# Kernel optimization log

Measured on AMD Instinct MI355X. Metric: run time of the kernel, lower is better.

Reference implementation:

```python
import jax, jax.numpy as jnp
import numpy as np

DIM = 512
B, H_GRID, W_GRID = 16, 64, 64
N_TOKENS = 1 + H_GRID * W_GRID


def setup_inputs() -> dict:
    key = jax.random.key(0)
    ks = jax.random.split(key, 7)
    x = jax.random.normal(ks[0], (B, N_TOKENS, DIM), dtype=jnp.float32)
    # depthwise conv weights, torch layout [C_out, C_in/groups=1, k, k]
    w7 = jax.random.normal(ks[1], (DIM, 1, 7, 7), dtype=jnp.float32) * 0.02
    b7 = jax.random.normal(ks[2], (DIM,), dtype=jnp.float32) * 0.02
    w5 = jax.random.normal(ks[3], (DIM, 1, 5, 5), dtype=jnp.float32) * 0.02
    b5 = jax.random.normal(ks[4], (DIM,), dtype=jnp.float32) * 0.02
    w3 = jax.random.normal(ks[5], (DIM, 1, 3, 3), dtype=jnp.float32) * 0.02
    b3 = jax.random.normal(ks[6], (DIM,), dtype=jnp.float32) * 0.02
    return {"x": x, "w7": w7, "b7": b7, "w5": w5, "b5": b5,
            "w3": w3, "b3": b3, "H": H_GRID, "W": W_GRID}


def _dwconv(v, w, b, k):
    # depthwise same-padding conv, NCHW / OIHW, feature_group_count = channels
    p = k // 2
    C = v.shape[1]
    y = jax.lax.conv_general_dilated(
        v, w, window_strides=(1, 1), padding=[(p, p), (p, p)],
        dimension_numbers=("NCHW", "OIHW", "NCHW"),
        feature_group_count=C)
    return y + b[None, :, None, None]


def reference(x, w7, b7, w5, b5, w3, b3, H, W):
    Bsz, N, C = x.shape
    cls_token = x[:, :1]                         # [B, 1, C]
    feat_tokens = x[:, 1:]                       # [B, H*W, C]
    cnn_feat = feat_tokens.transpose(0, 2, 1).reshape(Bsz, C, H, W)
    x_conv = (_dwconv(cnn_feat, w7, b7, 7)
              + _dwconv(cnn_feat, w5, b5, 5)
              + _dwconv(cnn_feat, w3, b3, 3)
              + cnn_feat)
    feats = x_conv.reshape(Bsz, C, H * W).transpose(0, 2, 1)  # [B, H*W, C]
    return jnp.concatenate((cls_token, feats), axis=1)
```

## Files before the change

kernel.cpp:

```cpp
#include <hip/hip_runtime.h>
#include <type_traits>

#define DIMC 512
#define NTOK 4097
#define GH 64
#define GW 64
#define TH 4
#define WT 4

template <int I, int N, typename F>
__device__ __forceinline__ void static_for(F&& f)
{
    if constexpr (I < N) {
        f(std::integral_constant<int, I>{});
        static_for<I + 1, N>(f);
    }
}

__global__ __launch_bounds__(256) void prep_kernel(
    const float* __restrict__ w7, const float* __restrict__ b7,
    const float* __restrict__ w5, const float* __restrict__ b5,
    const float* __restrict__ w3, const float* __restrict__ b3,
    float* __restrict__ wc, float* __restrict__ bc)
{
    int idx = blockIdx.x * 256 + threadIdx.x;
    if (idx < DIMC * 49) {
        int c = idx & (DIMC - 1);
        int t = idx >> 9;
        int dy = t / 7, dx = t - dy * 7;
        float v = w7[c * 49 + t];
        if (dy >= 1 && dy <= 5 && dx >= 1 && dx <= 5)
            v += w5[c * 25 + (dy - 1) * 5 + (dx - 1)];
        if (dy >= 2 && dy <= 4 && dx >= 2 && dx <= 4)
            v += w3[c * 9 + (dy - 2) * 3 + (dx - 2)];
        if (dy == 3 && dx == 3) v += 1.0f;
        wc[t * DIMC + c] = v;
    }
    if (idx < DIMC) bc[idx] = b7[idx] + b5[idx] + b3[idx];
}

__global__ __launch_bounds__(256) void cls_kernel(
    const float* __restrict__ x, float* __restrict__ out)
{
    int i = blockIdx.x * 256 + threadIdx.x;
    int b = i >> 9, c = i & 511;
    size_t off = (size_t)b * NTOK * DIMC + c;
    out[off] = x[off];
}

__global__ __launch_bounds__(256) void dwconv_kernel(
    const float* __restrict__ x, const float* __restrict__ wc,
    const float* __restrict__ bc, float* __restrict__ out)
{
    __shared__ float wt_lds[49 * 64];

    const int lane  = threadIdx.x;
    const int wtile = threadIdx.y;
    const int cs    = blockIdx.x;
    const int rs    = blockIdx.y & 15;
    const int cg    = blockIdx.y >> 4;
    const int b     = blockIdx.z;
    const int cc    = (cg << 6) + lane;
    const int h0    = rs * TH;
    const int w0    = cs * 16 + wtile * WT;

    for (int j = wtile * 64 + lane; j < 49 * 64; j += 256)
        wt_lds[j] = wc[(j >> 6) * DIMC + (cg << 6) + (j & 63)];
    __syncthreads();

    const float bias = bc[cc];
    const float* __restrict__ xin = x   + ((size_t)b * NTOK + 1) * DIMC + cc;
    float* __restrict__ op        = out + ((size_t)b * NTOK + 1) * DIMC + cc;

    float acc[TH][WT];

    static_for<0, TH + 6>([&](auto iC) {
        constexpr int i = decltype(iC)::value;
        const int r = h0 + (i - 3);

        float row[WT + 6];
        if (r >= 0 && r < GH) {
            const float* __restrict__ rp = xin + (size_t)r * (GW * DIMC);
            static_for<0, WT + 6>([&](auto jC) {
                constexpr int j = decltype(jC)::value;
                const int col = w0 - 3 + j;
                row[j] = (col >= 0 && col < GW) ? rp[(size_t)col * DIMC] : 0.0f;
            });
        } else {
            static_for<0, WT + 6>([&](auto jC) {
                row[decltype(jC)::value] = 0.0f;
            });
        }

        static_for<0, 7>([&](auto dyC) {
            constexpr int dy = decltype(dyC)::value;
            constexpr int k  = i - dy;
            if constexpr (k >= 0 && k < TH) {
                float wr[7];
                static_for<0, 7>([&](auto dxC) {
                    constexpr int dx = decltype(dxC)::value;
                    wr[dx] = wt_lds[(dy * 7 + dx) * 64 + lane];
                });
                static_for<0, WT>([&](auto tC) {
                    constexpr int t = decltype(tC)::value;
                    float a = (dy == 0) ? bias : acc[k][t];
#pragma unroll
                    for (int dx = 0; dx < 7; ++dx)
                        a = fmaf(wr[dx], row[t + dx], a);
                    acc[k][t] = a;
                });
            }
        });

        if constexpr (i >= 6) {
            constexpr int k = i - 6;
            static_for<0, WT>([&](auto tC) {
                constexpr int t = decltype(tC)::value;
                op[((size_t)(h0 + k) * GW + (w0 + t)) * DIMC] = acc[k][t];
            });
        }
    });
}

extern "C" void kernel_launch(void* const* d_in, const int* in_sizes, int n_in,
                              void* d_out, int out_size, void* d_ws, size_t ws_size,
                              hipStream_t stream)
{
    const float* x  = (const float*)d_in[0];
    const float* w7 = (const float*)d_in[1];
    const float* b7 = (const float*)d_in[2];
    const float* w5 = (const float*)d_in[3];
    const float* b5 = (const float*)d_in[4];
    const float* w3 = (const float*)d_in[5];
    const float* b3 = (const float*)d_in[6];
    float* out = (float*)d_out;
    float* wcomb = (float*)d_ws;
    float* bcomb = wcomb + 49 * DIMC;

    prep_kernel<<<98, 256, 0, stream>>>(w7, b7, w5, b5, w3, b3, wcomb, bcomb);
    cls_kernel<<<32, 256, 0, stream>>>(x, out);

    dim3 grid(4, 128, 16);
    dim3 block(64, 4, 1);
    dwconv_kernel<<<grid, block, 0, stream>>>(x, wcomb, bcomb, out);
}
```

Before: 296.9 us.

## Widen per-thread column tile, vectorize weight LDS reads, fuse cls copy into prep

```diff
diff --git a/kernel.cpp b/kernel.cpp
--- a/kernel.cpp
+++ b/kernel.cpp
@@ -6,7 +6,7 @@
 #define GH 64
 #define GW 64
 #define TH 4
-#define WT 4
+#define WT 8
 
 template <int I, int N, typename F>
 __device__ __forceinline__ void static_for(F&& f)
@@ -18,10 +18,12 @@
 }
 
 __global__ __launch_bounds__(256) void prep_kernel(
+    const float* __restrict__ x,
     const float* __restrict__ w7, const float* __restrict__ b7,
     const float* __restrict__ w5, const float* __restrict__ b5,
     const float* __restrict__ w3, const float* __restrict__ b3,
-    float* __restrict__ wc, float* __restrict__ bc)
+    float* __restrict__ wc, float* __restrict__ bc,
+    float* __restrict__ out)
 {
     int idx = blockIdx.x * 256 + threadIdx.x;
     if (idx < DIMC * 49) {
@@ -37,22 +39,19 @@
         wc[t * DIMC + c] = v;
     }
     if (idx < DIMC) bc[idx] = b7[idx] + b5[idx] + b3[idx];
-}
-
-__global__ __launch_bounds__(256) void cls_kernel(
-    const float* __restrict__ x, float* __restrict__ out)
-{
-    int i = blockIdx.x * 256 + threadIdx.x;
-    int b = i >> 9, c = i & 511;
-    size_t off = (size_t)b * NTOK * DIMC + c;
-    out[off] = x[off];
+    int cidx = idx - DIMC * 49;
+    if (cidx >= 0 && cidx < 16 * DIMC) {
+        int b = cidx >> 9, c = cidx & 511;
+        size_t off = (size_t)b * NTOK * DIMC + c;
+        out[off] = x[off];
+    }
 }
 
 __global__ __launch_bounds__(256) void dwconv_kernel(
     const float* __restrict__ x, const float* __restrict__ wc,
     const float* __restrict__ bc, float* __restrict__ out)
 {
-    __shared__ float wt_lds[49 * 64];
+    __shared__ __align__(16) float wt_lds[7 * 2 * 256];
 
     const int lane  = threadIdx.x;
     const int wtile = threadIdx.y;
@@ -62,10 +61,14 @@
     const int b     = blockIdx.z;
     const int cc    = (cg << 6) + lane;
     const int h0    = rs * TH;
-    const int w0    = cs * 16 + wtile * WT;
+    const int w0    = cs * 32 + wtile * WT;
 
-    for (int j = wtile * 64 + lane; j < 49 * 64; j += 256)
-        wt_lds[j] = wc[(j >> 6) * DIMC + (cg << 6) + (j & 63)];
+    for (int idx = wtile * 64 + lane; idx < 7 * 2 * 256; idx += 256) {
+        int chunk = idx >> 8, within = idx & 255;
+        int l = within >> 2, q = within & 3;
+        int dy = chunk >> 1, tap = (chunk & 1) * 4 + q;
+        wt_lds[idx] = (tap < 7) ? wc[(dy * 7 + tap) * DIMC + (cg << 6) + l] : 0.0f;
+    }
     __syncthreads();
 
     const float bias = bc[cc];
@@ -96,11 +99,11 @@
             constexpr int dy = decltype(dyC)::value;
             constexpr int k  = i - dy;
             if constexpr (k >= 0 && k < TH) {
-                float wr[7];
-                static_for<0, 7>([&](auto dxC) {
-                    constexpr int dx = decltype(dxC)::value;
-                    wr[dx] = wt_lds[(dy * 7 + dx) * 64 + lane];
-                });
+                const float4 wa = *reinterpret_cast<const float4*>(
+                    &wt_lds[(dy * 2 + 0) * 256 + (lane << 2)]);
+                const float4 wb = *reinterpret_cast<const float4*>(
+                    &wt_lds[(dy * 2 + 1) * 256 + (lane << 2)]);
+                const float wr[7] = {wa.x, wa.y, wa.z, wa.w, wb.x, wb.y, wb.z};
                 static_for<0, WT>([&](auto tC) {
                     constexpr int t = decltype(tC)::value;
                     float a = (dy == 0) ? bias : acc[k][t];
@@ -137,10 +140,10 @@
     float* wcomb = (float*)d_ws;
     float* bcomb = wcomb + 49 * DIMC;
 
-    prep_kernel<<<98, 256, 0, stream>>>(w7, b7, w5, b5, w3, b3, wcomb, bcomb);
-    cls_kernel<<<32, 256, 0, stream>>>(x, out);
+    prep_kernel<<<130, 256, 0, stream>>>(x, w7, b7, w5, b5, w3, b3,
+                                         wcomb, bcomb, out);
 
-    dim3 grid(4, 128, 16);
+    dim3 grid(2, 128, 16);
     dim3 block(64, 4, 1);
     dwconv_kernel<<<grid, block, 0, stream>>>(x, wcomb, bcomb, out);
 }
```

New measurement: 300.5 us. About the same (+1.2%).
